# Performance work log

Measured on AMD Instinct MI355X. Metric: run time of the kernel, lower is better.

Reference implementation:

```python
import jax, jax.numpy as jnp
import numpy as np

NUM_T = 1000
B, N = 16, 2048
M = 8192


def _cosine_alphas_cumprod(T=NUM_T, s=0.008):
    # Faithful to ColdDiffusion.cosine_beta_schedule + cumprod of (1 - betas)
    x = np.linspace(0.0, T, T + 1)
    ac = np.cos((x / T + s) / (1 + s) * np.pi * 0.5) ** 2
    ac = ac / ac[0]
    betas = np.clip(1.0 - ac[1:] / ac[:-1], 0.0001, 0.9999)
    return np.cumprod(1.0 - betas)


def setup_inputs() -> dict:
    key = jax.random.key(0)
    k1, k2, k3 = jax.random.split(key, 3)
    x_start = jax.random.normal(k1, (B, N, 4, 2), dtype=jnp.float32)
    anchors = jax.random.normal(k2, (M, 4, 2), dtype=jnp.float32)
    t = jax.random.randint(k3, (B,), 0, NUM_T)
    ac = _cosine_alphas_cumprod()
    sqrt_alphas_cumprod = jnp.asarray(np.sqrt(ac), dtype=jnp.float32)
    sqrt_one_minus_alphas_cumprod = jnp.asarray(np.sqrt(1.0 - ac), dtype=jnp.float32)
    return {
        "x_start": x_start,
        "anchors": anchors,
        "sqrt_alphas_cumprod": sqrt_alphas_cumprod,
        "sqrt_one_minus_alphas_cumprod": sqrt_one_minus_alphas_cumprod,
        "t": t,
    }


def reference(x_start, anchors, sqrt_alphas_cumprod, sqrt_one_minus_alphas_cumprod, t):
    # q_sample with anchor matching, fully batched (no Python loop over B).
    Bq, Nq = x_start.shape[:2]
    xf = x_start.reshape(Bq, Nq, -1)            # [B,N,8]
    af = anchors.reshape(anchors.shape[0], -1)  # [M,8]
    scores = jnp.einsum('bnd,md->bnm', xf, af) * (-2.0) + jnp.sum(af * af, axis=-1)  # [B,N,M]
    idx = jnp.argmin(scores, axis=-1)           # [B,N]
    matched = anchors[idx]                      # [B,N,4,2] gather
    sa = sqrt_alphas_cumprod[t][:, None, None, None]                 # [B,1,1,1]
    sb = sqrt_one_minus_alphas_cumprod[t][:, None, None, None]       # [B,1,1,1]
    return sa * x_start + sb * matched
```

## Files before the change

kernel.cpp:

```cpp
#include <hip/hip_runtime.h>
#include <stdint.h>

#define B_      16
#define N_      2048
#define M_      8192
#define ROWS    (B_ * N_)
#define D_      8

#define BLK     256
#define RPW     8
#define WPB     4
#define RPB     (RPW * WPB)
#define NBLK    (ROWS / RPB)
#define CHUNK   512
#define NCHUNK  (M_ / CHUNK)
#define STEPS   (CHUNK / 64)
#define PFPT    (CHUNK / BLK)

__device__ __forceinline__ float rfl(float v) {
    return __int_as_float(__builtin_amdgcn_readfirstlane(__float_as_int(v)));
}

__global__ __launch_bounds__(BLK, 4) void colddiff_kernel(
    const float* __restrict__ x,
    const float* __restrict__ anchors,
    const float* __restrict__ sa_tab,
    const float* __restrict__ sb_tab,
    const int*   __restrict__ t,
    float* __restrict__ out)
{
    __shared__ float4 sA0[CHUNK];
    __shared__ float4 sA1[CHUNK];
    __shared__ float  sH [CHUNK];

    const int tid  = threadIdx.x;
    const int lane = tid & 63;
    const int wave = tid >> 6;
    const int rowbase = blockIdx.x * RPB + wave * RPW;

    float Xs[RPW][D_];
    #pragma unroll
    for (int r = 0; r < RPW; ++r) {
        const float4* px = (const float4*)(x + (size_t)(rowbase + r) * D_);
        const float4 lo = px[0], hi = px[1];
        Xs[r][0] = rfl(-lo.x); Xs[r][1] = rfl(-lo.y);
        Xs[r][2] = rfl(-lo.z); Xs[r][3] = rfl(-lo.w);
        Xs[r][4] = rfl(-hi.x); Xs[r][5] = rfl(-hi.y);
        Xs[r][6] = rfl(-hi.z); Xs[r][7] = rfl(-hi.w);
    }

    float best[RPW];
    int   bidx[RPW];
    #pragma unroll
    for (int r = 0; r < RPW; ++r) { best[r] = 3.4e38f; bidx[r] = 0; }

    const float4* gA = (const float4*)anchors;
    float4 p0[PFPT], p1[PFPT];
    #pragma unroll
    for (int i = 0; i < PFPT; ++i) {
        const int slot = tid + i * BLK;
        p0[i] = gA[2 * slot];
        p1[i] = gA[2 * slot + 1];
    }

    for (int c = 0; c < NCHUNK; ++c) {
        __syncthreads();
        #pragma unroll
        for (int i = 0; i < PFPT; ++i) {
            const int slot = tid + i * BLK;
            const float4 a0 = p0[i], a1 = p1[i];
            float nr = a0.x * a0.x;
            nr = fmaf(a0.y, a0.y, nr);
            nr = fmaf(a0.z, a0.z, nr);
            nr = fmaf(a0.w, a0.w, nr);
            nr = fmaf(a1.x, a1.x, nr);
            nr = fmaf(a1.y, a1.y, nr);
            nr = fmaf(a1.z, a1.z, nr);
            nr = fmaf(a1.w, a1.w, nr);
            sA0[slot] = a0;
            sA1[slot] = a1;
            sH [slot] = 0.5f * nr;
        }
        __syncthreads();
        if (c + 1 < NCHUNK) {
            #pragma unroll
            for (int i = 0; i < PFPT; ++i) {
                const int slot = (c + 1) * CHUNK + tid + i * BLK;
                p0[i] = gA[2 * slot];
                p1[i] = gA[2 * slot + 1];
            }
        }
        #pragma unroll 2
        for (int k = 0; k < STEPS; ++k) {
            const int slot = k * 64 + lane;
            const float4 a0 = sA0[slot];
            const float4 a1 = sA1[slot];
            const float  hn = sH [slot];
            const int    j  = c * CHUNK + slot;
            #pragma unroll
            for (int r = 0; r < RPW; ++r) {
                float s = fmaf(Xs[r][0], a0.x, hn);
                s = fmaf(Xs[r][1], a0.y, s);
                s = fmaf(Xs[r][2], a0.z, s);
                s = fmaf(Xs[r][3], a0.w, s);
                s = fmaf(Xs[r][4], a1.x, s);
                s = fmaf(Xs[r][5], a1.y, s);
                s = fmaf(Xs[r][6], a1.z, s);
                s = fmaf(Xs[r][7], a1.w, s);
                const bool cc = s < best[r];
                best[r] = cc ? s : best[r];
                bidx[r] = cc ? j : bidx[r];
            }
        }
    }

    #pragma unroll
    for (int r = 0; r < RPW; ++r) {
        #pragma unroll
        for (int m = 1; m < 64; m <<= 1) {
            const float ov = __shfl_xor(best[r], m);
            const int   oj = __shfl_xor(bidx[r], m);
            const bool take = (ov < best[r]) || (ov == best[r] && oj < bidx[r]);
            best[r] = take ? ov : best[r];
            bidx[r] = take ? oj : bidx[r];
        }
    }

    if (lane < RPW) {
        int selj = bidx[0];
        #pragma unroll
        for (int r = 1; r < RPW; ++r) selj = (lane == r) ? bidx[r] : selj;

        const int row = rowbase + lane;
        const int tb  = t[row >> 11];
        const float sa = sa_tab[tb];
        const float sb = sb_tab[tb];

        const float4* px = (const float4*)(x + (size_t)row * D_);
        const float4* pa = (const float4*)(anchors + (size_t)selj * D_);
        const float4 x0 = px[0], x1 = px[1];
        const float4 a0 = pa[0], a1 = pa[1];

        float4 o0, o1;
        o0.x = fmaf(sa, x0.x, sb * a0.x);
        o0.y = fmaf(sa, x0.y, sb * a0.y);
        o0.z = fmaf(sa, x0.z, sb * a0.z);
        o0.w = fmaf(sa, x0.w, sb * a0.w);
        o1.x = fmaf(sa, x1.x, sb * a1.x);
        o1.y = fmaf(sa, x1.y, sb * a1.y);
        o1.z = fmaf(sa, x1.z, sb * a1.z);
        o1.w = fmaf(sa, x1.w, sb * a1.w);

        float4* po = (float4*)(out + (size_t)row * D_);
        po[0] = o0;
        po[1] = o1;
    }
}

extern "C" void kernel_launch(void* const* d_in, const int* in_sizes, int n_in,
                              void* d_out, int out_size, void* d_ws, size_t ws_size,
                              hipStream_t stream) {
    const float* x       = (const float*)d_in[0];
    const float* anchors = (const float*)d_in[1];
    const float* sa_tab  = (const float*)d_in[2];
    const float* sb_tab  = (const float*)d_in[3];
    const int*   t       = (const int*)d_in[4];
    float* out = (float*)d_out;

    colddiff_kernel<<<NBLK, BLK, 0, stream>>>(x, anchors, sa_tab, sb_tab, t, out);
}
```

Baseline: 128.8 us.

## Split anchor chunk across wave pairs and merge argmin via shared memory

Each block now handles 16 rows instead of 32. Two waves share each group of 8 rows, and each wave scans half of every anchor chunk. Partial argmin results are merged through shared memory with a tie-break on the lower index. This doubles the block count and raises the launch-bounds occupancy hint to 8, giving more parallelism and latency hiding, but each block now loads the full anchor set for half as many rows, so global and LDS staging traffic per row doubles.

```diff
diff --git a/kernel.cpp b/kernel.cpp
--- a/kernel.cpp
+++ b/kernel.cpp
@@ -9,19 +9,18 @@
 
 #define BLK     256
 #define RPW     8
-#define WPB     4
-#define RPB     (RPW * WPB)
+#define RPB     16
 #define NBLK    (ROWS / RPB)
 #define CHUNK   512
 #define NCHUNK  (M_ / CHUNK)
-#define STEPS   (CHUNK / 64)
+#define KSTEPS  4
 #define PFPT    (CHUNK / BLK)
 
 __device__ __forceinline__ float rfl(float v) {
     return __int_as_float(__builtin_amdgcn_readfirstlane(__float_as_int(v)));
 }
 
-__global__ __launch_bounds__(BLK, 4) void colddiff_kernel(
+__global__ __launch_bounds__(BLK, 8) void colddiff_kernel(
     const float* __restrict__ x,
     const float* __restrict__ anchors,
     const float* __restrict__ sa_tab,
@@ -32,11 +31,15 @@
     __shared__ float4 sA0[CHUNK];
     __shared__ float4 sA1[CHUNK];
     __shared__ float  sH [CHUNK];
+    __shared__ float  sV [4 * RPW];
+    __shared__ int    sI [4 * RPW];
 
-    const int tid  = threadIdx.x;
-    const int lane = tid & 63;
-    const int wave = tid >> 6;
-    const int rowbase = blockIdx.x * RPB + wave * RPW;
+    const int tid   = threadIdx.x;
+    const int lane  = tid & 63;
+    const int wave  = tid >> 6;
+    const int group = wave >> 1;
+    const int khalf = wave & 1;
+    const int rowbase = blockIdx.x * RPB + group * RPW;
 
     float Xs[RPW][D_];
     #pragma unroll
@@ -91,8 +94,8 @@
             }
         }
         #pragma unroll 2
-        for (int k = 0; k < STEPS; ++k) {
-            const int slot = k * 64 + lane;
+        for (int k = 0; k < KSTEPS; ++k) {
+            const int slot = khalf * (CHUNK / 2) + k * 64 + lane;
             const float4 a0 = sA0[slot];
             const float4 a1 = sA1[slot];
             const float  hn = sH [slot];
@@ -127,17 +130,36 @@
     }
 
     if (lane < RPW) {
-        int selj = bidx[0];
+        float selv = best[0];
+        int   selj = bidx[0];
         #pragma unroll
-        for (int r = 1; r < RPW; ++r) selj = (lane == r) ? bidx[r] : selj;
+        for (int r = 1; r < RPW; ++r) {
+            const bool m = (lane == r);
+            selv = m ? best[r] : selv;
+            selj = m ? bidx[r] : selj;
+        }
+        sV[wave * RPW + lane] = selv;
+        sI[wave * RPW + lane] = selj;
+    }
+    __syncthreads();
 
-        const int row = rowbase + lane;
+    if (tid < RPB) {
+        const int grp = tid >> 3;
+        const int r   = tid & 7;
+        const float vA = sV[(2 * grp) * RPW + r];
+        const int   iA = sI[(2 * grp) * RPW + r];
+        const float vB = sV[(2 * grp + 1) * RPW + r];
+        const int   iB = sI[(2 * grp + 1) * RPW + r];
+        const bool take = (vB < vA) || (vB == vA && iB < iA);
+        const int bi = take ? iB : iA;
+
+        const int row = blockIdx.x * RPB + tid;
         const int tb  = t[row >> 11];
         const float sa = sa_tab[tb];
         const float sb = sb_tab[tb];
 
         const float4* px = (const float4*)(x + (size_t)row * D_);
-        const float4* pa = (const float4*)(anchors + (size_t)selj * D_);
+        const float4* pa = (const float4*)(anchors + (size_t)bi * D_);
         const float4 x0 = px[0], x1 = px[1];
         const float4 a0 = pa[0], a1 = pa[1];
 
```

New measurement: 137.4 us. +6.6%, slower.
